# Kernel tuning notes

Hardware: AMD Instinct MI355X
Metric: run time of the kernel (lower is better)

## Reference

```python
import jax, jax.numpy as jnp
import numpy as np

B, T, C = 2, 2048, 1024
H, D = 16, 64
EPS = 1e-05
SCALE = 1.0 / np.sqrt(D)


def _rmsnorm(x, w):
    # normalize over last dim (head_dim)
    return w * (x * jax.lax.rsqrt(jnp.mean(x * x, axis=-1, keepdims=True) + EPS))


def setup_inputs() -> dict:
    key = jax.random.key(0)
    ks = jax.random.split(key, 8)
    x = jax.random.normal(ks[0], (B, T, C), dtype=jnp.float32)
    # causal mask, 1 = attend, 0 = masked
    attention_mask = jnp.tril(jnp.ones((T, T), dtype=jnp.int32))[None, None]
    s = 1.0 / np.sqrt(C)
    Wq = jax.random.normal(ks[1], (C, H * D), dtype=jnp.float32) * s
    Wk = jax.random.normal(ks[2], (C, H * D), dtype=jnp.float32) * s
    Wv = jax.random.normal(ks[3], (C, H * D), dtype=jnp.float32) * s
    Wo = jax.random.normal(ks[4], (H * D, C), dtype=jnp.float32) * s
    q_norm_w = jnp.ones((D,), dtype=jnp.float32)
    k_norm_w = jnp.ones((D,), dtype=jnp.float32)
    gate = jnp.ones((1, H, 1, 1), dtype=jnp.float32)
    return {"x": x, "attention_mask": attention_mask, "Wq": Wq, "Wk": Wk,
            "Wv": Wv, "Wo": Wo, "q_norm_w": q_norm_w, "k_norm_w": k_norm_w,
            "gate": gate}


def reference(x, attention_mask, Wq, Wk, Wv, Wo, q_norm_w, k_norm_w, gate):
    Bx, Tx, Cx = x.shape
    vx = x @ Wv                                   # [B,T,H*D] (kept for value residual)
    q = (x @ Wq).reshape(Bx, Tx, H, D).transpose(0, 2, 1, 3)  # [B,H,T,D]
    k = (x @ Wk).reshape(Bx, Tx, H, D).transpose(0, 2, 1, 3)
    v = vx.reshape(Bx, Tx, H, D).transpose(0, 2, 1, 3)
    q = _rmsnorm(q, q_norm_w)
    k = _rmsnorm(k, k_norm_w)
    att = jnp.einsum('bhqd,bhkd->bhqk', q, k) * SCALE
    att = jnp.where(attention_mask == 0, -jnp.inf, att)
    att = jax.nn.softmax(att, axis=-1)
    att = att * gate                              # per-head gating after softmax
    out = jnp.einsum('bhqk,bhkd->bhqd', att, v)
    out = out.transpose(0, 2, 1, 3).reshape(Bx, Tx, Cx)
    out = out + vx                                # value residual
    out = out @ Wo
    return out
```

## Files before the change

### kernel.cpp

```cpp
#include <hip/hip_runtime.h>

#define T_SEQ 2048
#define CDIM 1024
#define NHEAD 16
#define HDIM 64
#define BATCH 2
#define EPSV 1e-5f
#define SCALE 0.125f
#define LOG2E 1.44269504088896f
#define SMAX 16.0f

typedef __attribute__((ext_vector_type(8))) short bf16x8;
typedef __attribute__((ext_vector_type(4))) float f32x4;

__device__ __forceinline__ float b2f(short s) {
  unsigned u = ((unsigned)(unsigned short)s) << 16;
  return __builtin_bit_cast(float, u);
}
__device__ __forceinline__ short f2b(float f) {
  unsigned u = __builtin_bit_cast(unsigned, f);
  unsigned r = (u + 0x7fffu + ((u >> 16) & 1u)) >> 16;
  return (short)r;
}
__device__ __forceinline__ unsigned cvt_pk_bf16(float a, float b) {
  unsigned r;
  asm("v_cvt_pk_bf16_f32 %0, %1, %2" : "=v"(r) : "v"(a), "v"(b));
  return r;
}

__device__ __forceinline__ void gld16(const void* g, void* l) {
  __builtin_amdgcn_global_load_lds((const __attribute__((address_space(1))) unsigned*)g,
                                   (__attribute__((address_space(3))) unsigned*)l, 16, 0, 0);
}

__device__ __forceinline__ int gswz(int row) { return ((row >> 1) ^ (row >> 3)) & 3; }

__device__ __forceinline__ void stage_sw(short* lds, const char* gbase, int gstride,
                                         int w, int l) {
#pragma unroll
  for (int i = 0; i < 2; ++i) {
    int chunk = w * 2048 + i * 1024 + l * 16;
    int row = chunk >> 7;
    int bir = chunk & 127;
    const char* src = gbase + (size_t)row * gstride + (bir ^ ((row & 7) << 4));
    gld16(src, (char*)lds + chunk);
  }
}
__device__ __forceinline__ void stage_sw8(short* lds, const char* gbase, int gstride,
                                          int w, int l) {
  int chunk = w * 1024 + l * 16;
  int row = chunk >> 7;
  int bir = chunk & 127;
  const char* src = gbase + (size_t)row * gstride + (bir ^ ((row & 7) << 4));
  gld16(src, (char*)lds + chunk);
}

__global__ __launch_bounds__(256) void prep(const float* __restrict__ x,
                                            const float* __restrict__ Wq,
                                            const float* __restrict__ Wk,
                                            const float* __restrict__ Wv,
                                            const float* __restrict__ Wo,
                                            short* __restrict__ xb,
                                            short* __restrict__ WT) {
  __shared__ float tile[64][65];
  const int bid = blockIdx.x;
  if (bid < 2048) {
    size_t i = ((size_t)bid * 256 + threadIdx.x) * 8;
    float4 a = *(const float4*)&x[i];
    float4 b = *(const float4*)&x[i + 4];
    short4 lo, hi;
    lo.x = f2b(a.x); lo.y = f2b(a.y); lo.z = f2b(a.z); lo.w = f2b(a.w);
    hi.x = f2b(b.x); hi.y = f2b(b.y); hi.z = f2b(b.z); hi.w = f2b(b.w);
    *(short4*)&xb[i] = lo;
    *(short4*)&xb[i + 4] = hi;
    return;
  }
  const int t = bid - 2048;
  const int z = t >> 8, rem = t & 255;
  const float* W = (z == 0) ? Wq : (z == 1) ? Wk : (z == 2) ? Wv : Wo;
  const int r0 = (rem >> 4) * 64, c0 = (rem & 15) * 64;
  const int tr = threadIdx.x >> 4, tc4 = (threadIdx.x & 15) * 4;
#pragma unroll
  for (int i = 0; i < 4; ++i) {
    float4 v = *(const float4*)&W[(size_t)(r0 + tr + i * 16) * 1024 + c0 + tc4];
    tile[tr + i * 16][tc4 + 0] = v.x;
    tile[tr + i * 16][tc4 + 1] = v.y;
    tile[tr + i * 16][tc4 + 2] = v.z;
    tile[tr + i * 16][tc4 + 3] = v.w;
  }
  __syncthreads();
#pragma unroll
  for (int i = 0; i < 4; ++i) {
    int n = tr + i * 16;
    short4 o;
    o.x = f2b(tile[tc4 + 0][n]);
    o.y = f2b(tile[tc4 + 1][n]);
    o.z = f2b(tile[tc4 + 2][n]);
    o.w = f2b(tile[tc4 + 3][n]);
    *(short4*)&WT[((size_t)(z * 1024) + c0 + n) * 1024 + r0 + tc4] = o;
  }
}

template <int BN, bool F32OUT, bool NORM>
__global__ __launch_bounds__(256) void gemm_bf16(const short* __restrict__ A,
                                                 const short* __restrict__ Bt,
                                                 void* __restrict__ Cv,
                                                 const float* __restrict__ qw,
                                                 const float* __restrict__ kw,
                                                 int M, int N, int K, int nbx) {
  constexpr int NFR = BN / 32;
  constexpr int BITERS = BN / 64;
  __shared__ __attribute__((aligned(16))) short As[3][4096];
  __shared__ __attribute__((aligned(16))) short Bs[3][BN * 32];
  const int tid = threadIdx.x;
  const int w = tid >> 6, l = tid & 63;
  const int g = l >> 4, c = l & 15;
  const int wm = w >> 1, wn = w & 1;
  const int xcd = blockIdx.x & 7;
  const int i = blockIdx.x >> 3;
  const int bx = i >> 2;
  const int by = xcd * 4 + (i & 3);
  const int m0 = by * 128, n0 = bx * BN;
  const char* Ab = (const char*)A;
  const char* Bb = (const char*)Bt;

  auto stage = [&](int k0, int buf) {
#pragma unroll
    for (int ii = 0; ii < 2; ++ii) {
      int ci = w * 128 + ii * 64 + l;
      int row = ci >> 2, c4 = ci & 3;
      gld16(Ab + ((size_t)(m0 + row) * K + k0) * 2 + ((c4 ^ gswz(row)) << 4),
            (char*)As[buf] + (w * 2048 + ii * 1024));
    }
#pragma unroll
    for (int ii = 0; ii < BITERS; ++ii) {
      int ci = w * (64 * BITERS) + ii * 64 + l;
      int row = ci >> 2, c4 = ci & 3;
      gld16(Bb + ((size_t)(n0 + row) * K + k0) * 2 + ((c4 ^ gswz(row)) << 4),
            (char*)Bs[buf] + (w * (1024 * BITERS) + ii * 1024));
    }
  };

  f32x4 acc[4][NFR];
#pragma unroll
  for (int mt = 0; mt < 4; ++mt)
#pragma unroll
    for (int nt = 0; nt < NFR; ++nt) {
      f32x4 z = {0.f, 0.f, 0.f, 0.f};
      acc[mt][nt] = z;
    }

  const int NT = K >> 5;
  stage(0, 0);
  stage(32, 1);
  if constexpr (BITERS == 2) asm volatile("s_waitcnt vmcnt(4)" ::: "memory");
  else                       asm volatile("s_waitcnt vmcnt(3)" ::: "memory");
  __builtin_amdgcn_s_barrier();
  __builtin_amdgcn_sched_barrier(0);

  int cbuf = 0;
  for (int t = 0; t < NT; ++t) {
    int tgt = cbuf + 2; if (tgt >= 3) tgt -= 3;
    if (t + 2 < NT) stage((t + 2) << 5, tgt);
    bf16x8 a[4], bf[NFR];
#pragma unroll
    for (int mt = 0; mt < 4; ++mt) {
      const int row = wm * 64 + mt * 16 + c;
      a[mt] = *(const bf16x8*)&As[cbuf][row * 32 + ((g ^ gswz(row)) << 3)];
    }
#pragma unroll
    for (int nt = 0; nt < NFR; ++nt) {
      const int row = wn * (BN / 2) + nt * 16 + c;
      bf[nt] = *(const bf16x8*)&Bs[cbuf][row * 32 + ((g ^ gswz(row)) << 3)];
    }
    __builtin_amdgcn_s_setprio(1);
#pragma unroll
    for (int mt = 0; mt < 4; ++mt)
#pragma unroll
      for (int nt = 0; nt < NFR; ++nt)
        acc[mt][nt] = __builtin_amdgcn_mfma_f32_16x16x32_bf16(a[mt], bf[nt], acc[mt][nt], 0, 0, 0);
    __builtin_amdgcn_s_setprio(0);
    if (t + 1 < NT) {
      if (t + 2 < NT) {
        if constexpr (BITERS == 2) asm volatile("s_waitcnt vmcnt(4)" ::: "memory");
        else                       asm volatile("s_waitcnt vmcnt(3)" ::: "memory");
      } else {
        asm volatile("s_waitcnt vmcnt(0)" ::: "memory");
      }
      __builtin_amdgcn_s_barrier();
      __builtin_amdgcn_sched_barrier(0);
    }
    cbuf = cbuf + 1; if (cbuf >= 3) cbuf -= 3;
  }

  if constexpr (NORM) {
    if (n0 < 2048) {
      const float* wgt = (n0 < 1024) ? qw : kw;
      const float scl = (n0 < 1024) ? SCALE * LOG2E : 1.f;
      float w4[NFR];
#pragma unroll
      for (int nt = 0; nt < NFR; ++nt) w4[nt] = wgt[nt * 16 + c] * scl;
#pragma unroll
      for (int mt = 0; mt < 4; ++mt)
#pragma unroll
        for (int r = 0; r < 4; ++r) {
          float s = 0.f;
#pragma unroll
          for (int nt = 0; nt < NFR; ++nt) s += acc[mt][nt][r] * acc[mt][nt][r];
          s += __shfl_xor(s, 1);
          s += __shfl_xor(s, 2);
          s += __shfl_xor(s, 4);
          s += __shfl_xor(s, 8);
          const float rstd = rsqrtf(s * (1.0f / 64.0f) + EPSV);
#pragma unroll
          for (int nt = 0; nt < NFR; ++nt) acc[mt][nt][r] *= rstd * w4[nt];
        }
    }
  }

  if constexpr (F32OUT) {
    float* C = (float*)Cv;
#pragma unroll
    for (int mt = 0; mt < 4; ++mt)
#pragma unroll
      for (int nt = 0; nt < NFR; ++nt)
#pragma unroll
        for (int r = 0; r < 4; ++r)
          C[(size_t)(m0 + wm * 64 + mt * 16 + 4 * g + r) * N + n0 + wn * (BN / 2) + nt * 16 + c] =
              acc[mt][nt][r];
  } else {
    short* C = (short*)Cv;
#pragma unroll
    for (int mt = 0; mt < 4; ++mt)
#pragma unroll
      for (int nt = 0; nt < NFR; ++nt)
#pragma unroll
        for (int r = 0; r < 4; ++r)
          C[(size_t)(m0 + wm * 64 + mt * 16 + 4 * g + r) * N + n0 + wn * (BN / 2) + nt * 16 + c] =
              f2b(acc[mt][nt][r]);
  }
}

__global__ __launch_bounds__(256) void vt_kernel(const short* __restrict__ QKV,
                                                 short* __restrict__ VT) {
  __shared__ short tile[64][66];
  const int t0 = blockIdx.x * 64;
  const int h = blockIdx.y, b = blockIdx.z;
  const int tid = threadIdx.x;
  const int r = tid >> 3, c8 = (tid & 7) * 8;
#pragma unroll
  for (int p = 0; p < 2; ++p) {
    int row = r + p * 32;
    bf16x8 v = *(const bf16x8*)&QKV[(size_t)(b * T_SEQ + t0 + row) * 3072 + 2048 + h * 64 + c8];
#pragma unroll
    for (int j = 0; j < 8; ++j) tile[row][c8 + j] = v[j];
  }
  __syncthreads();
#pragma unroll
  for (int p = 0; p < 2; ++p) {
    int d = r + p * 32;
    short o[8];
#pragma unroll
    for (int j = 0; j < 8; ++j) o[j] = tile[c8 + j][d];
    *(bf16x8*)&VT[((size_t)(b * NHEAD + h) * 64 + d) * T_SEQ + t0 + c8] = *(bf16x8*)o;
  }
}

__global__ __launch_bounds__(512, 4) void attn_fwd(const short* __restrict__ QKV,
                                                   const short* __restrict__ VT,
                                                   const float* __restrict__ gate,
                                                   short* __restrict__ Ob) {
  __shared__ __attribute__((aligned(16))) short pool[32768];

  const int bid = blockIdx.x;
  const int xcd = bid & 7, s = bid >> 3;
  const int t8 = (s >> 2) & 7;
  const int Q16 = (s < 32) ? 15 - t8 : t8;
  const int bh = xcd * 4 + (s & 3);
  const int h = bh & 15, b = bh >> 4;
  const int q0 = Q16 * 128;
  const int nkt = 2 * Q16 + 2;
  const int tid = threadIdx.x;
  const int w = tid >> 6, l = tid & 63;
  const int g = l >> 4, c = l & 15;

  const char* qkb = (const char*)QKV;
  const char* kbase = qkb + ((size_t)(b * T_SEQ) * 3072 + 1024 + h * 64) * 2;
  const char* vtb = (const char*)VT + ((size_t)(b * NHEAD + h) * 64) * T_SEQ * 2;
  const float gh = gate[h];

  stage_sw(pool, qkb + ((size_t)(b * T_SEQ + q0) * 3072 + h * 64) * 2, 3072 * 2, w, l);
  stage_sw8(pool + 8192, kbase, 3072 * 2, w, l);
  stage_sw8(pool + 20480, vtb, T_SEQ * 2, w, l);
  stage_sw8(pool + 8192 + 4096, kbase + (size_t)64 * 3072 * 2, 3072 * 2, w, l);
  stage_sw8(pool + 20480 + 4096, vtb + (size_t)64 * 2, T_SEQ * 2, w, l);
  asm volatile("s_waitcnt vmcnt(4)" ::: "memory");
  __builtin_amdgcn_sched_barrier(0);

  bf16x8 qf[2];
  {
    const int row = w * 16 + c;
#pragma unroll
    for (int ks = 0; ks < 2; ++ks)
      qf[ks] = *(const bf16x8*)&pool[row * 64 + ((ks * 32 + g * 8) ^ ((row & 7) << 3))];
  }

  const char* poolb = (const char*)pool;
  const int bc = (c >> 2) & 1;
  const int swz_g = (g ^ (c & 3)) << 4;
  const int kvoff[2] = {c * 128 + swz_g + (bc << 6),
                        c * 128 + swz_g + ((1 ^ bc) << 6)};
  const int pboff[2] = {w * 2048 + kvoff[0], w * 2048 + kvoff[1]};
  const int cc = (c >> 1) & 3;
  const int pinv = w * 2048 + c * 128 + ((g & 1) << 3) + ((((g >> 1) ^ c) & 1) << 4);
  int p_off[4];
#pragma unroll
  for (int mt = 0; mt < 4; ++mt) p_off[mt] = pinv + ((mt ^ cc) << 5);

  bf16x8 onesf;
#pragma unroll
  for (int j = 0; j < 8; ++j) onesf[j] = (short)0x3F80;

  f32x4 oacc[4];
#pragma unroll
  for (int dt = 0; dt < 4; ++dt) {
    f32x4 z = {0.f, 0.f, 0.f, 0.f};
    oacc[dt] = z;
  }
  f32x4 oacc4 = {0.f, 0.f, 0.f, 0.f};

#define ATTN_BODY(BUF_, KT_)                                                              \
  {                                                                                       \
    constexpr int BUF = (BUF_);                                                           \
    const int kt = (KT_);                                                                 \
    if (kt + 1 < nkt) asm volatile("s_waitcnt vmcnt(2)" ::: "memory");                    \
    else              asm volatile("s_waitcnt vmcnt(0)" ::: "memory");                    \
    __builtin_amdgcn_s_barrier();                                                         \
    __builtin_amdgcn_sched_barrier(0);                                                    \
    if (kt + 2 < nkt) {                                                                   \
      constexpr int TGT = (BUF + 2) % 3;                                                  \
      stage_sw8(pool + 8192 + TGT * 4096, kbase + (size_t)(kt + 2) * 64 * 3072 * 2,       \
                3072 * 2, w, l);                                                          \
      stage_sw8(pool + 20480 + TGT * 4096, vtb + (size_t)(kt + 2) * 64 * 2,               \
                T_SEQ * 2, w, l);                                                         \
    }                                                                                     \
    const int dq = q0 + w * 16 - kt * 64;                                                 \
    if (dq > -16) {                                                                       \
      f32x4 sacc[4];                                                                      \
      _Pragma("unroll") for (int mt = 0; mt < 4; ++mt) {                                  \
        f32x4 z = {-SMAX, -SMAX, -SMAX, -SMAX};                                           \
        sacc[mt] = z;                                                                     \
      }                                                                                   \
      __builtin_amdgcn_s_setprio(1);                                                      \
      _Pragma("unroll") for (int mt = 0; mt < 4; ++mt) {                                  \
        _Pragma("unroll") for (int ks = 0; ks < 2; ++ks) {                                \
          bf16x8 kf = *(const bf16x8*)(poolb + 16384 + BUF * 8192 + mt * 2048 +           \
                                       kvoff[ks]);                                        \
          sacc[mt] = __builtin_amdgcn_mfma_f32_16x16x32_bf16(kf, qf[ks], sacc[mt],        \
                                                             0, 0, 0);                    \
        }                                                                                 \
      }                                                                                   \
      __builtin_amdgcn_s_setprio(0);                                                      \
      bf16x8 vf[4][2];                                                                    \
      _Pragma("unroll") for (int dt = 0; dt < 4; ++dt)                                    \
        _Pragma("unroll") for (int ks = 0; ks < 2; ++ks)                                  \
          vf[dt][ks] = *(const bf16x8*)(poolb + 40960 + BUF * 8192 + dt * 2048 +          \
                                        kvoff[ks]);                                       \
      if (dq < 63) {                                                                      \
        _Pragma("unroll") for (int mt = 0; mt < 4; ++mt)                                  \
          _Pragma("unroll") for (int r = 0; r < 4; ++r)                                   \
            if (mt * 16 + 4 * g + r > dq + c) sacc[mt][r] = -1e30f;                       \
      }                                                                                   \
      _Pragma("unroll") for (int mt = 0; mt < 4; ++mt) {                                  \
        float p0 = exp2f(sacc[mt][0]);                                                    \
        float p1 = exp2f(sacc[mt][1]);                                                    \
        float p2 = exp2f(sacc[mt][2]);                                                    \
        float p3 = exp2f(sacc[mt][3]);                                                    \
        uint2 pk;                                                                         \
        pk.x = cvt_pk_bf16(p0, p1);                                                       \
        pk.y = cvt_pk_bf16(p2, p3);                                                       \
        *(uint2*)((char*)pool + p_off[mt]) = pk;                                          \
      }                                                                                   \
      bf16x8 pb[2];                                                                       \
      _Pragma("unroll") for (int ks = 0; ks < 2; ++ks)                                    \
        pb[ks] = *(const bf16x8*)(poolb + pboff[ks]);                                     \
      __builtin_amdgcn_s_setprio(1);                                                      \
      _Pragma("unroll") for (int dt = 0; dt < 4; ++dt)                                    \
        _Pragma("unroll") for (int ks = 0; ks < 2; ++ks)                                  \
          oacc[dt] = __builtin_amdgcn_mfma_f32_16x16x32_bf16(vf[dt][ks], pb[ks],          \
                                                             oacc[dt], 0, 0, 0);          \
      oacc4 = __builtin_amdgcn_mfma_f32_16x16x32_bf16(onesf, pb[0], oacc4, 0, 0, 0);      \
      oacc4 = __builtin_amdgcn_mfma_f32_16x16x32_bf16(onesf, pb[1], oacc4, 0, 0, 0);      \
      __builtin_amdgcn_s_setprio(0);                                                      \
    }                                                                                     \
  }

  int base = 0;
  for (; base + 3 <= nkt; base += 3) {
    ATTN_BODY(0, base);
    ATTN_BODY(1, base + 1);
    ATTN_BODY(2, base + 2);
  }
  if (base < nkt) ATTN_BODY(0, base);
  if (base + 1 < nkt) ATTN_BODY(1, base + 1);
#undef ATTN_BODY

  const float gl = gh / oacc4[0];
  const int qrow = q0 + w * 16 + c;
  const short* Vr = QKV + (size_t)(b * T_SEQ + qrow) * 3072 + 2048 + h * 64;
  short* Oro = Ob + (size_t)(b * T_SEQ + qrow) * 1024 + h * 64;
#pragma unroll
  for (int dt = 0; dt < 4; ++dt) {
    const int d0 = dt * 16 + 4 * g;
    short4 vres = *(const short4*)&Vr[d0];
    short4 o;
    o.x = f2b(oacc[dt][0] * gl + b2f(vres.x));
    o.y = f2b(oacc[dt][1] * gl + b2f(vres.y));
    o.z = f2b(oacc[dt][2] * gl + b2f(vres.z));
    o.w = f2b(oacc[dt][3] * gl + b2f(vres.w));
    *(short4*)&Oro[d0] = o;
  }
}

extern "C" void kernel_launch(void* const* d_in, const int* in_sizes, int n_in,
                              void* d_out, int out_size, void* d_ws, size_t ws_size,
                              hipStream_t stream) {
  const float* x  = (const float*)d_in[0];
  const float* Wq = (const float*)d_in[2];
  const float* Wk = (const float*)d_in[3];
  const float* Wv = (const float*)d_in[4];
  const float* Wo = (const float*)d_in[5];
  const float* qw = (const float*)d_in[6];
  const float* kw = (const float*)d_in[7];
  const float* gate = (const float*)d_in[8];
  float* out = (float*)d_out;

  char* ws = (char*)d_ws;
  short* xb  = (short*)ws;
  short* WT  = (short*)(ws + ((size_t)8 << 20));
  short* QKV = (short*)(ws + ((size_t)16 << 20));
  short* VTb = (short*)(ws + ((size_t)40 << 20));
  short* Obf = (short*)(ws + ((size_t)48 << 20));

  const int M = BATCH * T_SEQ;

  prep<<<3072, 256, 0, stream>>>(x, Wq, Wk, Wv, Wo, xb, WT);
  gemm_bf16<128, false, true><<<768, 256, 0, stream>>>(xb, WT, QKV, qw, kw, M, 3072, CDIM, 24);
  vt_kernel<<<dim3(32, 16, 2), 256, 0, stream>>>(QKV, VTb);
  attn_fwd<<<512, 512, 0, stream>>>(QKV, VTb, gate, Obf);
  gemm_bf16<64, true, false><<<512, 256, 0, stream>>>(Obf, WT + (size_t)3072 * 1024, out,
                                                      nullptr, nullptr, M, CDIM, CDIM, 16);
}
```

Baseline: 109.7 us.

## Process KV tiles in pairs with four-buffer LDS ring and one barrier per pair

Restructures the attention K/V pipeline from a triple-buffered one-tile-per-barrier loop to a four-slot ring. Each barrier now prefetches two tiles at once and the block computes two tiles before waiting again. This halves the number of waitcnt/barrier synchronisations per block. In exchange, LDS use per block grows from 64KB to 80KB, which may reduce occupancy below the launch-bounds target. The full vmcnt(0) wait before each pair may also expose more load latency.

```diff
diff --git a/kernel.cpp b/kernel.cpp
--- a/kernel.cpp
+++ b/kernel.cpp
@@ -270,7 +270,7 @@
                                                    const short* __restrict__ VT,
                                                    const float* __restrict__ gate,
                                                    short* __restrict__ Ob) {
-  __shared__ __attribute__((aligned(16))) short pool[32768];
+  __shared__ __attribute__((aligned(16))) short pool[40960];
 
   const int bid = blockIdx.x;
   const int xcd = bid & 7, s = bid >> 3;
@@ -291,9 +291,9 @@
 
   stage_sw(pool, qkb + ((size_t)(b * T_SEQ + q0) * 3072 + h * 64) * 2, 3072 * 2, w, l);
   stage_sw8(pool + 8192, kbase, 3072 * 2, w, l);
-  stage_sw8(pool + 20480, vtb, T_SEQ * 2, w, l);
+  stage_sw8(pool + 24576, vtb, T_SEQ * 2, w, l);
   stage_sw8(pool + 8192 + 4096, kbase + (size_t)64 * 3072 * 2, 3072 * 2, w, l);
-  stage_sw8(pool + 20480 + 4096, vtb + (size_t)64 * 2, T_SEQ * 2, w, l);
+  stage_sw8(pool + 24576 + 4096, vtb + (size_t)64 * 2, T_SEQ * 2, w, l);
   asm volatile("s_waitcnt vmcnt(4)" ::: "memory");
   __builtin_amdgcn_sched_barrier(0);
 
@@ -329,21 +329,10 @@
   }
   f32x4 oacc4 = {0.f, 0.f, 0.f, 0.f};
 
-#define ATTN_BODY(BUF_, KT_)                                                              \
+#define ATTN_TILE(BUF_, KT_)                                                              \
   {                                                                                       \
     constexpr int BUF = (BUF_);                                                           \
     const int kt = (KT_);                                                                 \
-    if (kt + 1 < nkt) asm volatile("s_waitcnt vmcnt(2)" ::: "memory");                    \
-    else              asm volatile("s_waitcnt vmcnt(0)" ::: "memory");                    \
-    __builtin_amdgcn_s_barrier();                                                         \
-    __builtin_amdgcn_sched_barrier(0);                                                    \
-    if (kt + 2 < nkt) {                                                                   \
-      constexpr int TGT = (BUF + 2) % 3;                                                  \
-      stage_sw8(pool + 8192 + TGT * 4096, kbase + (size_t)(kt + 2) * 64 * 3072 * 2,       \
-                3072 * 2, w, l);                                                          \
-      stage_sw8(pool + 20480 + TGT * 4096, vtb + (size_t)(kt + 2) * 64 * 2,               \
-                T_SEQ * 2, w, l);                                                         \
-    }                                                                                     \
     const int dq = q0 + w * 16 - kt * 64;                                                 \
     if (dq > -16) {                                                                       \
       f32x4 sacc[4];                                                                      \
@@ -364,7 +353,7 @@
       bf16x8 vf[4][2];                                                                    \
       _Pragma("unroll") for (int dt = 0; dt < 4; ++dt)                                    \
         _Pragma("unroll") for (int ks = 0; ks < 2; ++ks)                                  \
-          vf[dt][ks] = *(const bf16x8*)(poolb + 40960 + BUF * 8192 + dt * 2048 +          \
+          vf[dt][ks] = *(const bf16x8*)(poolb + 49152 + BUF * 8192 + dt * 2048 +          \
                                         kvoff[ks]);                                       \
       if (dq < 63) {                                                                      \
         _Pragma("unroll") for (int mt = 0; mt < 4; ++mt)                                  \
@@ -395,15 +384,36 @@
     }                                                                                     \
   }
 
-  int base = 0;
-  for (; base + 3 <= nkt; base += 3) {
-    ATTN_BODY(0, base);
-    ATTN_BODY(1, base + 1);
-    ATTN_BODY(2, base + 2);
-  }
-  if (base < nkt) ATTN_BODY(0, base);
-  if (base + 1 < nkt) ATTN_BODY(1, base + 1);
-#undef ATTN_BODY
+#define ATTN_PAIR(B_, T0_)                                                                \
+  {                                                                                       \
+    constexpr int PB = (B_);                                                              \
+    const int pt0 = (T0_);                                                                \
+    asm volatile("s_waitcnt vmcnt(0)" ::: "memory");                                      \
+    __builtin_amdgcn_s_barrier();                                                         \
+    __builtin_amdgcn_sched_barrier(0);                                                    \
+    if (pt0 + 2 < nkt) {                                                                  \
+      constexpr int TB = PB ^ 2;                                                          \
+      stage_sw8(pool + 8192 + TB * 4096, kbase + (size_t)(pt0 + 2) * 64 * 3072 * 2,       \
+                3072 * 2, w, l);                                                          \
+      stage_sw8(pool + 24576 + TB * 4096, vtb + (size_t)(pt0 + 2) * 64 * 2,               \
+                T_SEQ * 2, w, l);                                                         \
+      stage_sw8(pool + 8192 + (TB + 1) * 4096, kbase + (size_t)(pt0 + 3) * 64 * 3072 * 2, \
+                3072 * 2, w, l);                                                          \
+      stage_sw8(pool + 24576 + (TB + 1) * 4096, vtb + (size_t)(pt0 + 3) * 64 * 2,         \
+                T_SEQ * 2, w, l);                                                         \
+    }                                                                                     \
+    ATTN_TILE(PB, pt0);                                                                   \
+    ATTN_TILE(PB + 1, pt0 + 1);                                                           \
+  }
+
+  int t0 = 0;
+  for (; t0 + 4 <= nkt; t0 += 4) {
+    ATTN_PAIR(0, t0);
+    ATTN_PAIR(2, t0 + 2);
+  }
+  if (t0 < nkt) ATTN_PAIR(0, t0);
+#undef ATTN_PAIR
+#undef ATTN_TILE
 
   const float gl = gh / oacc4[0];
   const int qrow = q0 + w * 16 + c;
```

Result: no change. 109.7 us (+0.0%).
